# Optimization experiments

Measured on AMD Instinct MI355X. Metric: run time of the kernel, lower is better.

Reference implementation:

```python
import math
import jax, jax.numpy as jnp
import numpy as np

N, C, H, W = 8, 128, 112, 112
# frozen random.randint shifts from __init__
S7_01, S8_10 = 2, -1          # roll along dim1 (c), dim3 (h)
S11_11, S12_10, S12_11, S13_11 = 1, -1, 0, 1  # rolls along dim4 (w) / dim3 (h)


def _conv(x, w, padding, rhs_dilation=(1, 1), groups=1):
    return jax.lax.conv_general_dilated(
        x, w, window_strides=(1, 1), padding=padding,
        lhs_dilation=(1, 1), rhs_dilation=rhs_dilation,
        dimension_numbers=('NCHW', 'OIHW', 'NCHW'),
        feature_group_count=groups)


def setup_inputs() -> dict:
    key = jax.random.key(0)
    ks = jax.random.split(key, 6)
    x = jax.random.normal(ks[0], (N, C, H, W), jnp.float32)
    w3 = jax.random.normal(ks[1], (C, C, 1, 3), jnp.float32) * 0.02   # Conv2d(c,c,(1,3),dil=(1,2),pad=(0,2))
    w4 = jax.random.normal(ks[2], (C, 1, 7, 1), jnp.float32) * 0.02   # depthwise Conv2d(c,c,(7,1),dil=(3,1),pad=(9,0),groups=c)
    w9 = jax.random.normal(ks[3], (1, C, C), jnp.float32) * 0.02      # p_9_w
    w10 = jax.random.normal(ks[4], (1, C, 7, 1, 1), jnp.float32) * 0.02  # p_10_w
    w15 = jax.random.normal(ks[5], (C, C * 7 // 4, 1, 1), jnp.float32) * 0.02  # Conv2d(c*7,c,1,groups=4)
    return {"x": x, "w3": w3, "w4": w4, "w9": w9, "w10": w10, "w15": w15}


def reference(x, w3, w4, w9, w10, w15):
    n, c, h, w = x.shape
    hw = h * w
    t1 = jax.nn.sigmoid(x)
    t2 = t1 * x                                   # SiLU
    t3 = _conv(t2, w3, ((0, 0), (2, 2)), rhs_dilation=(1, 2))
    t4 = _conv(t3, w4, ((9, 9), (0, 0)), rhs_dilation=(3, 1), groups=c)
    # channel attention: bmm(t1, t0^T) / sqrt(h*w) -> (n,c,c)
    t5 = jnp.einsum('ncs,nds->ncd', t1.reshape(n, c, hw), x.reshape(n, c, hw)) / math.sqrt(hw)
    # F.unfold(t4, (7,1), dilation=(2,1), padding=(6,0)) -> (n,c,7,h,w)
    padded = jnp.pad(t4, ((0, 0), (0, 0), (6, 6), (0, 0)))
    t6 = jnp.stack([padded[:, :, 2 * k:2 * k + h, :] for k in range(7)], axis=2)
    t7 = jnp.roll(t6, S7_01, axis=1)
    t8 = jnp.roll(t7, S8_10, axis=3)
    t9 = w9 * t5
    t10 = w10 * t8
    t11 = jnp.roll(t10, S11_11, axis=4)
    t12 = jnp.roll(jnp.roll(t11, S12_10, axis=3), S12_11, axis=4)
    t13 = jnp.roll(t12, S13_11, axis=4)
    # bmm(t9^T, t2) / sqrt(c): out[n,d,s] = sum_c t9[n,c,d] * t2[n,c,s]
    t14 = (jnp.einsum('ncd,ncs->nds', t9, t2.reshape(n, c, hw)) / math.sqrt(c)).reshape(n, c, h, w)
    t15 = _conv(t13.reshape(n, c * 7, h, w), w15, ((0, 0), (0, 0)), groups=4)
    return t15 + t14
```

## Files before the change

kernel.cpp:

```cpp
#include <hip/hip_runtime.h>
#include <hip/hip_bf16.h>

#define NB 8
#define CC 128
#define HH 112
#define WW 112
#define HWS (HH*WW)
#define PLANE (CC*HWS)
#define TOT (NB*PLANE)
#define XP 116
#define LROW 130
#define PLANEP ((size_t)HH*XP*CC)

typedef __attribute__((ext_vector_type(8))) short short8v;
typedef __attribute__((ext_vector_type(4))) float float4v;

__device__ __forceinline__ float bflo(unsigned u){ return __uint_as_float(u<<16); }
__device__ __forceinline__ float bfhi(unsigned u){ return __uint_as_float(u & 0xffff0000u); }
__device__ __forceinline__ float ldv(const float* p, size_t i){ return p[i]; }
__device__ __forceinline__ float ldv(const ushort* p, size_t i){ return __uint_as_float(((unsigned)p[i])<<16); }
__device__ __forceinline__ void ld8(const ushort* p, float* v){
    uint4 u0 = *((const uint4*)p);
    v[0]=bflo(u0.x); v[1]=bfhi(u0.x); v[2]=bflo(u0.y); v[3]=bfhi(u0.y);
    v[4]=bflo(u0.z); v[5]=bfhi(u0.z); v[6]=bflo(u0.w); v[7]=bfhi(u0.w);
}
__device__ __forceinline__ void ld8(const float* p, float* v){
    float4 a = *((const float4*)p); float4 b = *((const float4*)(p+4));
    v[0]=a.x; v[1]=a.y; v[2]=a.z; v[3]=a.w; v[4]=b.x; v[5]=b.y; v[6]=b.z; v[7]=b.w;
}
__device__ __forceinline__ void ld4(const float* p, float* v){
    float4 a = *((const float4*)p);
    v[0]=a.x; v[1]=a.y; v[2]=a.z; v[3]=a.w;
}
__device__ __forceinline__ void ld4(const ushort* p, float* v){
    uint2 u = *((const uint2*)p);
    v[0]=bflo(u.x); v[1]=bfhi(u.x); v[2]=bflo(u.y); v[3]=bfhi(u.y);
}
__device__ __forceinline__ ushort f2bf(float f){
    unsigned u = __float_as_uint(f);
    return (ushort)((u + 0x7fffu + ((u>>16)&1u)) >> 16);
}
__device__ __forceinline__ void stv(float* o, size_t i, float v){ o[i]=v; }
__device__ __forceinline__ void stv(ushort* o, size_t i, float v){ o[i]=f2bf(v); }

__global__ __launch_bounds__(256) void detect_k(const ushort* __restrict__ x, int* __restrict__ flag){
    __shared__ int cnt;
    if (threadIdx.x==0) cnt = 0;
    __syncthreads();
    int bad = 0;
    for (int i = threadIdx.x; i < 2048; i += 256){
        float v = ldv(x, i);
        if (!(v > -1e4f && v < 1e4f)) bad++;
    }
    atomicAdd(&cnt, bad);
    __syncthreads();
    if (threadIdx.x==0) *flag = (cnt > 64) ? 1 : 0;
}

template<typename ET>
__device__ __forceinline__ void wpack_body(const ET* __restrict__ w3, ushort* __restrict__ Wpk){
    int idx = blockIdx.x*256 + threadIdx.x;
    if (idx < CC*384){
        int o = idx/384, kap = idx - o*384;
        int k = kap>>7, i = kap&127;
        Wpk[idx] = f2bf(ldv(w3, (o*128+i)*3 + k));
    }
}
__global__ __launch_bounds__(256) void wpack_k(const void* w3, ushort* Wpk, const int* fl){
    if (*fl) wpack_body((const float*)w3, Wpk); else wpack_body((const ushort*)w3, Wpk);
}

template<typename ET>
__device__ __forceinline__ void bpad_body(const ET* __restrict__ x, ushort* __restrict__ Bpad){
    int y = blockIdx.x, n = blockIdx.y;
    __shared__ ushort px[XP*LROW];
    const ET* xb = x + (size_t)n*PLANE + y*WW;
    for (int idx=threadIdx.x; idx<CC*28; idx+=256){
        int i = idx/28, xq = (idx - i*28)*4;
        float v[4]; ld4(xb + (size_t)i*HWS + xq, v);
        #pragma unroll
        for (int d=0;d<4;d++){
            float vv = v[d];
            float sv = vv * (1.f/(1.f+expf(-vv)));
            px[(xq+d+2)*LROW + i] = f2bf(sv);
        }
    }
    for (int idx=threadIdx.x; idx<4*CC; idx+=256){
        int j = idx >> 7, i = idx & 127;
        int xp = (j<2) ? j : j+112;
        px[xp*LROW + i] = 0;
    }
    __syncthreads();
    ushort* ob = Bpad + ((size_t)n*HH + y)*XP*CC;
    for (int idx=threadIdx.x; idx<XP*16; idx+=256){
        int xp = idx >> 4, c8 = idx & 15;
        const ushort* pr = px + xp*LROW + c8*8;
        uint4 v;
        v.x = *((const uint*)(pr+0));
        v.y = *((const uint*)(pr+2));
        v.z = *((const uint*)(pr+4));
        v.w = *((const uint*)(pr+6));
        *((uint4*)(ob + (size_t)xp*CC + c8*8)) = v;
    }
}
__global__ __launch_bounds__(256) void bpad_k(const void* x, ushort* Bpad, const int* fl){
    if (*fl) bpad_body((const float*)x, Bpad); else bpad_body((const ushort*)x, Bpad);
}

__global__ __launch_bounds__(256) void conv3mm_k(const ushort* __restrict__ Bpad, const ushort* __restrict__ Wpk,
                                                 ushort* __restrict__ t3T){
    int bx = blockIdx.x;
    int n  = blockIdx.y;
    int sbi = bx >> 1, oh = bx & 1;
    int wid = threadIdx.x >> 6, lane = threadIdx.x & 63;
    int l15 = lane & 15, quad = lane >> 4;
    __shared__ ushort Alds[24576];
    {
        const int tid = threadIdx.x;
        uint4 tmp[12];
        #pragma unroll
        for (int it=0; it<12; it++){
            int g = it*256 + tid;
            int kcmt = g >> 6, sl = (g>>2)&15, sq = g&3;
            int kc = kcmt >> 2, mt = kcmt & 3;
            tmp[it] = *((const uint4*)(Wpk + (size_t)(oh*64 + mt*16 + sl)*384 + kc*32 + sq*8));
        }
        #pragma unroll
        for (int it=0; it<12; it++){
            int g = it*256 + tid;
            *((uint4*)(Alds + g*8)) = tmp[it];
        }
    }
    __syncthreads();

    int s0 = sbi*128 + wid*32;
    int s1 = s0 + l15, s2 = s1 + 16;
    int y1 = s1/WW, x1 = s1 - y1*WW;
    int y2 = s2/WW, x2 = s2 - y2*WW;
    const ushort* bb = Bpad + (size_t)n*PLANEP;
    const ushort* b1p = bb + ((size_t)y1*XP + x1)*CC + quad*8;
    const ushort* b2p = bb + ((size_t)y2*XP + x2)*CC + quad*8;
    const ushort* al = Alds + l15*32 + quad*8;

    float4v acc[4][2] = {};
    short8v BA[2][4], BB[2][4], a0[4], a1[4];

    auto ldb = [&](int g, short8v (&B)[2][4]){
        #pragma unroll
        for (int m=0;m<4;m++){
            B[0][m] = *((const short8v*)(b1p + g*256 + m*32));
            B[1][m] = *((const short8v*)(b2p + g*256 + m*32));
        }
    };
    auto lda = [&](int kc, short8v (&dst)[4]){
        #pragma unroll
        for (int mt=0;mt<4;mt++) dst[mt] = *((const short8v*)(al + (kc*4+mt)*512));
    };
    auto step = [&](const short8v (&a)[4], const short8v (&B)[2][4], int m){
        #pragma unroll
        for (int mt=0;mt<4;mt++){
            acc[mt][0] = __builtin_amdgcn_mfma_f32_16x16x32_bf16(a[mt], B[0][m], acc[mt][0],0,0,0);
            acc[mt][1] = __builtin_amdgcn_mfma_f32_16x16x32_bf16(a[mt], B[1][m], acc[mt][1],0,0,0);
        }
    };

    ldb(0, BA); lda(0, a0);
    ldb(1, BB);
    lda(1, a1);  step(a0, BA, 0);
    lda(2, a0);  step(a1, BA, 1);
    lda(3, a1);  step(a0, BA, 2);
    lda(4, a0);  step(a1, BA, 3);
    ldb(2, BA);
    lda(5, a1);  step(a0, BB, 0);
    lda(6, a0);  step(a1, BB, 1);
    lda(7, a1);  step(a0, BB, 2);
    lda(8, a0);  step(a1, BB, 3);
    lda(9, a1);  step(a0, BA, 0);
    lda(10, a0); step(a1, BA, 1);
    lda(11, a1); step(a0, BA, 2);
                 step(a1, BA, 3);

    ushort* tb = t3T + (size_t)n*PLANE;
    #pragma unroll
    for (int nt=0; nt<2; nt++){
        int s = s0 + nt*16 + l15;
        ushort* rowp = tb + (size_t)s*128 + oh*64 + quad*4;
        #pragma unroll
        for (int mt=0; mt<4; mt++){
            ushort4 v;
            v.x = f2bf(acc[mt][nt][0]); v.y = f2bf(acc[mt][nt][1]);
            v.z = f2bf(acc[mt][nt][2]); v.w = f2bf(acc[mt][nt][3]);
            *((ushort4*)(rowp + mt*16)) = v;
        }
    }
}

template<typename ET>
__device__ __forceinline__ void wdpack_body(const ET* __restrict__ w4, float* __restrict__ wdp){
    int idx = blockIdx.x*256 + threadIdx.x;
    if (idx < 896){ int k = idx >> 7, c = idx & 127; wdp[idx] = ldv(w4, c*7 + k); }
}
__global__ __launch_bounds__(256) void wdpack_k(const void* w4, float* wdp, const int* fl){
    if (*fl) wdpack_body((const float*)w4, wdp); else wdpack_body((const ushort*)w4, wdp);
}

__global__ __launch_bounds__(256) void dwconvT_k(const ushort* __restrict__ t3T, const float* __restrict__ wdp,
                                                 ushort* __restrict__ t4T){
    int by = blockIdx.x, n = blockIdx.y;
    int y = (by>>3) + (by&7)*14;
    const ushort* tb = t3T + (size_t)n*PLANE;
    ushort* ob = t4T + (size_t)n*PLANE + (size_t)y*WW*128;
    for (int it = threadIdx.x; it < WW*16; it += 256){
        int c8 = it & 15, x = it >> 4;
        int coff = c8*8;
        float acc8[8] = {0.f,0.f,0.f,0.f,0.f,0.f,0.f,0.f};
        #pragma unroll
        for (int k=0;k<7;k++){
            int row = y - 9 + 3*k;
            if (row < 0 || row >= HH) continue;
            float v[8]; ld8(tb + ((size_t)row*WW + x)*128 + coff, v);
            const float* wp = wdp + k*128 + coff;
            #pragma unroll
            for (int j=0;j<8;j++) acc8[j] = fmaf(wp[j], v[j], acc8[j]);
        }
        ushort tmp[8];
        #pragma unroll
        for (int j=0;j<8;j++) tmp[j] = f2bf(acc8[j]);
        *((short8v*)(ob + (size_t)x*128 + coff)) = *((const short8v*)tmp);
    }
}

template<typename ET>
__device__ __forceinline__ void fusew_body(const ET* __restrict__ w10, const ET* __restrict__ w15,
                                           ushort* __restrict__ Wfb){
    int idx = blockIdx.x*256+threadIdx.x;
    if (idx < CC*224){
        int o = idx / 224, r = idx - o*224;
        int g = o >> 5;
        int cl = r/7, k = r - cl*7;
        int c = g*32 + cl;
        Wfb[idx] = f2bf(ldv(w15, o*224 + r) * ldv(w10, c*7+k));
    }
}
__global__ __launch_bounds__(256) void fusew_k(const void* w10, const void* w15, ushort* Wfb, const int* fl){
    if (*fl) fusew_body((const float*)w10, (const float*)w15, Wfb);
    else     fusew_body((const ushort*)w10, (const ushort*)w15, Wfb);
}

__global__ __launch_bounds__(256) void wfapack_k(const ushort* __restrict__ Wfb, ushort* __restrict__ Wfa){
    int idx = blockIdx.x*256 + threadIdx.x;
    if (idx >= 57344) return;
    int j   = idx & 31;
    int l15 = (idx >> 5) & 15;
    int mt  = (idx >> 9) & 1;
    int q   = (idx >> 10) & 1;
    int k   = (idx >> 11) % 7;
    int w   = idx / 14336;
    int o = w*32 + mt*16 + l15;
    int cl = -1;
    if (q==1){ if (j < 30) cl = j + 2; }
    else     { if (j >= 30) cl = j - 30; }
    Wfa[idx] = (cl >= 0) ? Wfb[o*224 + cl*7 + k] : (ushort)0;
}

template<int ST0, int NST>
__device__ __forceinline__ void t15_body(const ushort* __restrict__ tbase, const ushort* __restrict__ Wfa,
                                         ushort* __restrict__ ub, int y, int w, int l15, int quad){
    int qlo = (w+3)&3;
    float4v acc[NST][2] = {};
    const ushort* xbase = tbase + ((size_t)(ST0*16) + l15)*128 + quad*8;

    auto ldrow = [&](int k, short8v (&B)[NST][2]){
        int row = y + 2*k - 6;
        const ushort* rbase = xbase + (size_t)row*WW*128;
        #pragma unroll
        for (int st=0; st<NST; st++){
            const ushort* bp = rbase + st*16*128;
            B[st][0] = *((const short8v*)(bp + qlo*32));
            B[st][1] = *((const short8v*)(bp + w*32));
        }
    };
    auto ldA = [&](int k, short8v (&A)[4]){
        const ushort* af = Wfa + (w*7 + k)*2048 + l15*32 + quad*8;
        A[0] = *((const short8v*)(af));
        A[1] = *((const short8v*)(af + 512));
        A[2] = *((const short8v*)(af + 1024));
        A[3] = *((const short8v*)(af + 1536));
    };
    auto domm = [&](const short8v (&A)[4], const short8v (&B)[NST][2]){
        #pragma unroll
        for (int st=0; st<NST; st++){
            acc[st][0] = __builtin_amdgcn_mfma_f32_16x16x32_bf16(A[0], B[st][0], acc[st][0], 0,0,0);
            acc[st][1] = __builtin_amdgcn_mfma_f32_16x16x32_bf16(A[1], B[st][0], acc[st][1], 0,0,0);
            acc[st][0] = __builtin_amdgcn_mfma_f32_16x16x32_bf16(A[2], B[st][1], acc[st][0], 0,0,0);
            acc[st][1] = __builtin_amdgcn_mfma_f32_16x16x32_bf16(A[3], B[st][1], acc[st][1], 0,0,0);
        }
    };

    if (y >= 6 && y <= 105){
        short8v BA[NST][2], BB[NST][2], A0[4], A1[4];
        ldrow(0, BA); ldrow(1, BB);
        ldA(0, A0);              domm(A0, BA);
        ldrow(2, BA); ldA(1, A1); domm(A1, BB);
        ldrow(3, BB); ldA(2, A0); domm(A0, BA);
        ldrow(4, BA); ldA(3, A1); domm(A1, BB);
        ldrow(5, BB); ldA(4, A0); domm(A0, BA);
        ldrow(6, BA); ldA(5, A1); domm(A1, BB);
                      ldA(6, A0); domm(A0, BA);
    } else {
        int klo = (y >= 6) ? 0 : ((7 - y) >> 1);
        int khi = min(6, (117 - y) >> 1);
        for (int k = klo; k <= khi; k++){
            short8v B[NST][2], A[4];
            ldrow(k, B); ldA(k, A); domm(A, B);
        }
    }

    #pragma unroll
    for (int st=0; st<NST; st++){
        int s = (ST0 + st)*16 + l15;
        #pragma unroll
        for (int mt=0; mt<2; mt++)
            #pragma unroll
            for (int r=0;r<4;r++)
                ub[(size_t)(mt*16+quad*4+r)*HWS + s] = f2bf(acc[st][mt][r]);
    }
}
__global__ __launch_bounds__(256) void t15v3_k(const ushort* __restrict__ t4T, const ushort* __restrict__ Wfa,
                                               ushort* __restrict__ u){
    int bx = blockIdx.x, n = blockIdx.y;
    int xh = bx & 1, byi = bx >> 1;
    int y = (byi>>3) + (byi&7)*14;
    int w = threadIdx.x >> 6, lane = threadIdx.x & 63;
    int l15 = lane & 15, quad = lane >> 4;
    const ushort* tbase = t4T + (size_t)n*PLANE;
    ushort* ub = u + ((size_t)n*CC + w*32)*HWS + (size_t)y*WW;
    if (xh == 0) t15_body<0,4>(tbase, Wfa, ub, y, w, l15, quad);
    else         t15_body<4,3>(tbase, Wfa, ub, y, w, l15, quad);
}

template<typename ET>
__device__ __forceinline__ void t5mm_body(const ET* __restrict__ x, float* __restrict__ t5){
    int ks = blockIdx.x, n = blockIdx.y;
    int wid = threadIdx.x>>6, lane = threadIdx.x&63;
    int l15 = lane&15, quad = lane>>4;
    const ET* xn = x + (size_t)n*PLANE;
    float4v acc[2][8] = {};
    for (int t=0; t<8; t++){
        int sb = ks*256 + t*32 + quad*8;
        short8v afr[2];
        #pragma unroll
        for (int mt=0; mt<2; mt++){
            int row = wid*32 + mt*16 + l15;
            float v[8]; ld8(xn + (size_t)row*HWS + sb, v);
            ushort tmp[8];
            #pragma unroll
            for (int j=0;j<8;j++) tmp[j] = f2bf(1.f/(1.f+expf(-v[j])));
            afr[mt] = *((const short8v*)tmp);
        }
        #pragma unroll
        for (int nt=0; nt<8; nt++){
            int row = nt*16 + l15;
            float v[8]; ld8(xn + (size_t)row*HWS + sb, v);
            ushort tmp[8];
            #pragma unroll
            for (int j=0;j<8;j++) tmp[j] = f2bf(v[j]);
            short8v bfr = *((const short8v*)tmp);
            acc[0][nt] = __builtin_amdgcn_mfma_f32_16x16x32_bf16(afr[0], bfr, acc[0][nt], 0,0,0);
            acc[1][nt] = __builtin_amdgcn_mfma_f32_16x16x32_bf16(afr[1], bfr, acc[1][nt], 0,0,0);
        }
    }
    float* t5n = t5 + n*16384;
    #pragma unroll
    for (int mt=0; mt<2; mt++){
        #pragma unroll
        for (int nt=0; nt<8; nt++){
            #pragma unroll
            for (int r=0; r<4; r++){
                int ci = wid*32 + mt*16 + quad*4 + r;
                int cj = nt*16 + l15;
                atomicAdd(&t5n[ci*128 + cj], acc[mt][nt][r]);
            }
        }
    }
}
__global__ __launch_bounds__(256) void t5mm_k(const void* x, float* t5, const int* fl){
    if (*fl) t5mm_body((const float*)x, t5); else t5mm_body((const ushort*)x, t5);
}

template<typename ET>
__device__ __forceinline__ void coefb_body(const ET* __restrict__ w9, const float* __restrict__ t5,
                                           ushort* __restrict__ coefb){
    const float sc = 7.89181775e-4f;
    int idx = blockIdx.x*256 + threadIdx.x;
    int n = idx >> 14, rem = idx & 16383;
    int d = rem >> 7, c = rem & 127;
    coefb[idx] = f2bf(ldv(w9, c*128 + d) * t5[n*16384 + c*128 + d] * sc);
}
__global__ __launch_bounds__(256) void coefb_k(const void* w9, const float* t5, ushort* coefb, const int* fl){
    if (*fl) coefb_body((const float*)w9, t5, coefb); else coefb_body((const ushort*)w9, t5, coefb);
}

template<typename OT>
__device__ __forceinline__ void final2_body(const ushort* __restrict__ Bpad, const ushort* __restrict__ coefb,
                                            const ushort* __restrict__ u, OT* __restrict__ out){
    int sb = blockIdx.x, n = blockIdx.y;
    int wid = threadIdx.x>>6, lane = threadIdx.x&63;
    int l15 = lane&15, quad = lane>>4;
    int shalf = wid >> 1, ohalf = wid & 1;
    int s0 = sb*64 + shalf*32;
    int s1 = s0 + l15, s2 = s1 + 16;
    int y1 = s1/WW, x1 = s1 - y1*WW;
    int y2 = s2/WW, x2 = s2 - y2*WW;
    const ushort* bb = Bpad + (size_t)n*PLANEP;
    const ushort* b1p = bb + ((size_t)y1*XP + x1 + 2)*CC + quad*8;
    const ushort* b2p = bb + ((size_t)y2*XP + x2 + 2)*CC + quad*8;
    const ushort* abase = coefb + (size_t)n*16384 + (size_t)(ohalf*64 + l15)*128 + quad*8;
    float4v acc[4][2] = {};
    short8v bv0[4], bv1[4], aP[4], aQ[4];
    #pragma unroll
    for (int kc=0;kc<4;kc++){
        bv0[kc] = *((const short8v*)(b1p + kc*32));
        bv1[kc] = *((const short8v*)(b2p + kc*32));
    }
    auto lda = [&](int kc, short8v (&dst)[4]){
        #pragma unroll
        for (int mt=0;mt<4;mt++) dst[mt] = *((const short8v*)(abase + mt*16*128 + kc*32));
    };
    auto step = [&](const short8v (&a)[4], int kc){
        #pragma unroll
        for (int mt=0;mt<4;mt++){
            acc[mt][0] = __builtin_amdgcn_mfma_f32_16x16x32_bf16(a[mt], bv0[kc], acc[mt][0],0,0,0);
            acc[mt][1] = __builtin_amdgcn_mfma_f32_16x16x32_bf16(a[mt], bv1[kc], acc[mt][1],0,0,0);
        }
    };
    lda(0, aP);
    lda(1, aQ); step(aP, 0);
    lda(2, aP); step(aQ, 1);
    lda(3, aQ); step(aP, 2);
                step(aQ, 3);
    #pragma unroll
    for (int mt=0; mt<4; mt++){
        #pragma unroll
        for (int nt=0; nt<2; nt++){
            int s = s0 + nt*16 + l15;
            int y = s/WW, xx = s - y*WW;
            int ys = y+2; if (ys>=HH) ys-=HH;
            int xs = xx-2; if (xs<0) xs+=WW;
            #pragma unroll
            for (int r=0; r<4; r++){
                int d = ohalf*64 + mt*16 + quad*4 + r;
                float val = ldv(u, ((size_t)n*CC+d)*HWS + ys*WW + xs) + acc[mt][nt][r];
                stv(out, ((size_t)n*CC+d)*HWS + s, val);
            }
        }
    }
}
__global__ __launch_bounds__(256) void final2_k(const ushort* Bpad, const ushort* coefb,
                                                const ushort* u, void* out, const int* fl){
    if (*fl) final2_body(Bpad, coefb, u, (float*)out);
    else     final2_body(Bpad, coefb, u, (ushort*)out);
}

extern "C" void kernel_launch(void* const* d_in, const int* in_sizes, int n_in,
                              void* d_out, int out_size, void* d_ws, size_t ws_size,
                              hipStream_t stream) {
    const void* x   = d_in[0];
    const void* w3  = d_in[1];
    const void* w4  = d_in[2];
    const void* w9  = d_in[3];
    const void* w10 = d_in[4];
    const void* w15 = d_in[5];

    ushort* t3T  = (ushort*)d_ws;
    ushort* u    = t3T;
    ushort* t4T  = t3T + TOT;
    ushort* Bpad = t4T + TOT;
    float*  t5   = (float*)(Bpad + NB*PLANEP);
    ushort* coefb= (ushort*)(t5 + NB*CC*CC);
    ushort* Wfb  = coefb + NB*CC*CC;
    ushort* Wpk  = Wfb + CC*224;
    ushort* Wfa  = Wpk + CC*384;
    float*  wdp  = (float*)(Wfa + 57344);
    int* flag    = (int*)(wdp + 896);

    detect_k<<<1, 256, 0, stream>>>((const ushort*)x, flag);
    hipMemsetAsync(t5, 0, NB*CC*CC*sizeof(float), stream);

    wpack_k  <<<192, 256, 0, stream>>>(w3, Wpk, flag);
    fusew_k  <<<112, 256, 0, stream>>>(w10, w15, Wfb, flag);
    wfapack_k<<<224, 256, 0, stream>>>(Wfb, Wfa);
    wdpack_k <<<4,   256, 0, stream>>>(w4, wdp, flag);
    bpad_k   <<<dim3(HH,NB), 256, 0, stream>>>(x, Bpad, flag);
    conv3mm_k<<<dim3(196,NB), 256, 0, stream>>>(Bpad, Wpk, t3T);
    dwconvT_k<<<dim3(HH,NB), 256, 0, stream>>>(t3T, wdp, t4T);
    t5mm_k   <<<dim3(49,NB), 256, 0, stream>>>(x, t5, flag);
    coefb_k  <<<NB*CC*CC/256, 256, 0, stream>>>(w9, t5, coefb, flag);
    t15v3_k  <<<dim3(224,NB), 256, 0, stream>>>(t4T, Wfa, u);
    final2_k <<<dim3(196,NB), 256, 0, stream>>>(Bpad, coefb, u, d_out, flag);
}
```

Baseline: 335.7 us.

## Stage t15 B operand rows through triple-buffered swizzled LDS

Rewrites the grouped 1x1 conv (t15) kernel so each row's activation tile is loaded cooperatively with coalesced uint4 loads into a triple-buffered, XOR-swizzled LDS ring. Loads run two k-steps ahead and weight fragments one step ahead, overlapping with the MFMAs. Before, each wave fetched its B fragments directly from global memory, so the four waves loaded overlapping data redundantly. The change adds 48KB of LDS per block and a barrier per k-step, which may reduce occupancy and add sync overhead.

```diff
diff --git a/kernel.cpp b/kernel.cpp
--- a/kernel.cpp
+++ b/kernel.cpp
@@ -264,56 +264,72 @@
 }
 
 template<int ST0, int NST>
-__device__ __forceinline__ void t15_body(const ushort* __restrict__ tbase, const ushort* __restrict__ Wfa,
-                                         ushort* __restrict__ ub, int y, int w, int l15, int quad){
+__device__ __forceinline__ void t15_body_v4(const ushort* __restrict__ tbase, const ushort* __restrict__ Wfa,
+                                            ushort* __restrict__ ub, int y, int w, int l15, int quad,
+                                            ushort* lds){
     int qlo = (w+3)&3;
+    int tid = threadIdx.x;
     float4v acc[NST][2] = {};
-    const ushort* xbase = tbase + ((size_t)(ST0*16) + l15)*128 + quad*8;
-
-    auto ldrow = [&](int k, short8v (&B)[NST][2]){
-        int row = y + 2*k - 6;
-        const ushort* rbase = xbase + (size_t)row*WW*128;
-        #pragma unroll
-        for (int st=0; st<NST; st++){
-            const ushort* bp = rbase + st*16*128;
-            B[st][0] = *((const short8v*)(bp + qlo*32));
-            B[st][1] = *((const short8v*)(bp + w*32));
-        }
-    };
-    auto ldA = [&](int k, short8v (&A)[4]){
+    int klo = (y >= 6) ? 0 : ((7 - y) >> 1);
+    int khi = min(6, (117 - y) >> 1);
+    int nk = khi - klo;
+
+    uint4 rg[NST];
+    auto issueB = [&](int k){
+        const ushort* rs = tbase + ((size_t)(y + 2*k - 6)*WW + ST0*16)*128;
+        #pragma unroll
+        for (int j=0;j<NST;j++) rg[j] = *((const uint4*)(rs + (size_t)(j*256+tid)*8));
+    };
+    auto writeB = [&](int bufi){
+        ushort* lb = lds + bufi*8192;
+        #pragma unroll
+        for (int j=0;j<NST;j++){
+            int g = j*256+tid;
+            int gp = g ^ ((g>>4)&7);
+            *((uint4*)(lb + gp*8)) = rg[j];
+        }
+    };
+    short8v A0[4], A1[4];
+    auto issueA = [&](int k, short8v (&A)[4]){
         const ushort* af = Wfa + (w*7 + k)*2048 + l15*32 + quad*8;
         A[0] = *((const short8v*)(af));
         A[1] = *((const short8v*)(af + 512));
         A[2] = *((const short8v*)(af + 1024));
         A[3] = *((const short8v*)(af + 1536));
     };
-    auto domm = [&](const short8v (&A)[4], const short8v (&B)[NST][2]){
+    auto domm = [&](int bufi, const short8v (&A)[4]){
+        const ushort* lb = lds + bufi*8192;
         #pragma unroll
         for (int st=0; st<NST; st++){
-            acc[st][0] = __builtin_amdgcn_mfma_f32_16x16x32_bf16(A[0], B[st][0], acc[st][0], 0,0,0);
-            acc[st][1] = __builtin_amdgcn_mfma_f32_16x16x32_bf16(A[1], B[st][0], acc[st][1], 0,0,0);
-            acc[st][0] = __builtin_amdgcn_mfma_f32_16x16x32_bf16(A[2], B[st][1], acc[st][0], 0,0,0);
-            acc[st][1] = __builtin_amdgcn_mfma_f32_16x16x32_bf16(A[3], B[st][1], acc[st][1], 0,0,0);
-        }
-    };
-
-    if (y >= 6 && y <= 105){
-        short8v BA[NST][2], BB[NST][2], A0[4], A1[4];
-        ldrow(0, BA); ldrow(1, BB);
-        ldA(0, A0);              domm(A0, BA);
-        ldrow(2, BA); ldA(1, A1); domm(A1, BB);
-        ldrow(3, BB); ldA(2, A0); domm(A0, BA);
-        ldrow(4, BA); ldA(3, A1); domm(A1, BB);
-        ldrow(5, BB); ldA(4, A0); domm(A0, BA);
-        ldrow(6, BA); ldA(5, A1); domm(A1, BB);
-                      ldA(6, A0); domm(A0, BA);
-    } else {
-        int klo = (y >= 6) ? 0 : ((7 - y) >> 1);
-        int khi = min(6, (117 - y) >> 1);
-        for (int k = klo; k <= khi; k++){
-            short8v B[NST][2], A[4];
-            ldrow(k, B); ldA(k, A); domm(A, B);
-        }
+            int xl = st*16 + l15;
+            int g0 = xl*16 + qlo*4 + quad;  g0 ^= (g0>>4)&7;
+            int g1 = xl*16 + w*4   + quad;  g1 ^= (g1>>4)&7;
+            short8v B0 = *((const short8v*)(lb + g0*8));
+            short8v B1 = *((const short8v*)(lb + g1*8));
+            acc[st][0] = __builtin_amdgcn_mfma_f32_16x16x32_bf16(A[0], B0, acc[st][0], 0,0,0);
+            acc[st][1] = __builtin_amdgcn_mfma_f32_16x16x32_bf16(A[1], B0, acc[st][1], 0,0,0);
+            acc[st][0] = __builtin_amdgcn_mfma_f32_16x16x32_bf16(A[2], B1, acc[st][0], 0,0,0);
+            acc[st][1] = __builtin_amdgcn_mfma_f32_16x16x32_bf16(A[3], B1, acc[st][1], 0,0,0);
+        }
+    };
+    auto iter = [&](int i, short8v (&Acur)[4], short8v (&Anx)[4]){
+        int kk = klo + i;
+        if (i+2 <= nk) issueB(kk+2);
+        if (i+1 <= nk) issueA(kk+1, Anx);
+        __builtin_amdgcn_sched_barrier(0);
+        domm(i%3, Acur);
+        if (i+2 <= nk) writeB((i+2)%3);
+        if (i < nk) __syncthreads();
+    };
+
+    issueB(klo);   writeB(0);
+    issueB(klo+1); writeB(1);
+    issueA(klo, A0);
+    __syncthreads();
+
+    for (int i=0; i<=nk; i+=2){
+        iter(i, A0, A1);
+        if (i+1 <= nk) iter(i+1, A1, A0);
     }
 
     #pragma unroll
@@ -326,8 +342,9 @@
                 ub[(size_t)(mt*16+quad*4+r)*HWS + s] = f2bf(acc[st][mt][r]);
     }
 }
-__global__ __launch_bounds__(256) void t15v3_k(const ushort* __restrict__ t4T, const ushort* __restrict__ Wfa,
+__global__ __launch_bounds__(256) void t15v4_k(const ushort* __restrict__ t4T, const ushort* __restrict__ Wfa,
                                                ushort* __restrict__ u){
+    __shared__ ushort lds[3*8192];
     int bx = blockIdx.x, n = blockIdx.y;
     int xh = bx & 1, byi = bx >> 1;
     int y = (byi>>3) + (byi&7)*14;
@@ -335,8 +352,8 @@
     int l15 = lane & 15, quad = lane >> 4;
     const ushort* tbase = t4T + (size_t)n*PLANE;
     ushort* ub = u + ((size_t)n*CC + w*32)*HWS + (size_t)y*WW;
-    if (xh == 0) t15_body<0,4>(tbase, Wfa, ub, y, w, l15, quad);
-    else         t15_body<4,3>(tbase, Wfa, ub, y, w, l15, quad);
+    if (xh == 0) t15_body_v4<0,4>(tbase, Wfa, ub, y, w, l15, quad, lds);
+    else         t15_body_v4<4,3>(tbase, Wfa, ub, y, w, l15, quad, lds);
 }
 
 template<typename ET>
@@ -496,6 +513,6 @@
     dwconvT_k<<<dim3(HH,NB), 256, 0, stream>>>(t3T, wdp, t4T);
     t5mm_k   <<<dim3(49,NB), 256, 0, stream>>>(x, t5, flag);
     coefb_k  <<<NB*CC*CC/256, 256, 0, stream>>>(w9, t5, coefb, flag);
-    t15v3_k  <<<dim3(224,NB), 256, 0, stream>>>(t4T, Wfa, u);
+    t15v4_k  <<<dim3(224,NB), 256, 0, stream>>>(t4T, Wfa, u);
     final2_k <<<dim3(196,NB), 256, 0, stream>>>(Bpad, coefb, u, d_out, flag);
 }
```

After: 327.6 us. 2.4% less time.
